# Optimization experiments

Measured on AMD Instinct MI355X. Metric: run time of the kernel, lower is better.

The kernel has to match this reference:

```python
import jax, jax.numpy as jnp
import numpy as np

B, S, H, I, E, K = 2, 2048, 1024, 2816, 8, 2


def setup_inputs() -> dict:
    key = jax.random.key(0)
    k1, k2, k3, k4, k5 = jax.random.split(key, 5)
    std = 0.02
    x = jax.random.normal(k1, (B, S, H), dtype=jnp.float32)
    gate_w = jax.random.normal(k2, (H, E), dtype=jnp.float32) * std   # router Linear(H,E), no bias
    Wg = jax.random.normal(k3, (E, H, I), dtype=jnp.float32) * std    # per-expert gate_proj
    Wu = jax.random.normal(k4, (E, H, I), dtype=jnp.float32) * std    # per-expert up_proj
    Wd = jax.random.normal(k5, (E, I, H), dtype=jnp.float32) * std    # per-expert down_proj
    return {"x": x, "gate_w": gate_w, "Wg": Wg, "Wu": Wu, "Wd": Wd}


def reference(x, gate_w, Wg, Wu, Wd):
    b, s, h = x.shape
    e = gate_w.shape[1]
    # --- Gating ---
    logits = jnp.einsum('bsh,he->bse', x, gate_w)                      # [B,S,E]
    top_vals, top_idx = jax.lax.top_k(logits, K)                       # [B,S,K]
    sel = (top_idx[..., None] == jnp.arange(e)).any(axis=-2)           # [B,S,E] bool, top-k mask
    sparse_logits = jnp.where(sel, logits, -jnp.inf)
    sparse_probs = jax.nn.softmax(sparse_logits, axis=-1)              # zero weight off top-k
    # --- Experts (dense over E, weighted by sparse probs; math identical to gather/scatter loop) ---
    xf = x.reshape(-1, h)                                              # [T,H], T=B*S
    g = jnp.einsum('th,ehi->tei', xf, Wg)                              # [T,E,I]
    u = jnp.einsum('th,ehi->tei', xf, Wu)
    act = jax.nn.silu(g) * u                                           # SwiGLU
    expert_out = jnp.einsum('tei,eih->teh', act, Wd)                   # [T,E,H]
    out = jnp.einsum('teh,te->th', expert_out, sparse_probs.reshape(-1, e))
    final_outputs = out.reshape(b, s, h)
    gate_logit = logits.reshape(-1, e)                                 # [B*S,E]
    return final_outputs, gate_logit
```

## Files before the change

### kernel.cpp

```cpp
#include <hip/hip_runtime.h>


namespace {
constexpr int TOKS = 4096;
constexpr int HDIM = 1024;
constexpr int IDIM = 2816;
constexpr int NEXP = 8;
constexpr int NROW = 8192;

constexpr size_t WGT_OFF = 0;
constexpr size_t WUT_OFF = 46137344;
constexpr size_t WDT_OFF = 92274688;
constexpr size_t A_OFF   = 138412032;
constexpr size_t ACT_OFF = 155189248;
constexpr size_t CNT_OFF = 201326592;
constexpr size_t OFS_OFF = CNT_OFF + 64;
constexpr size_t CUR_OFF = CNT_OFF + 128;
constexpr size_t TIX_OFF = CNT_OFF + 1024;
constexpr size_t TPR_OFF = TIX_OFF + 32768;
constexpr size_t SLT_OFF = TPR_OFF + 32768;
constexpr size_t PRT_OFF = 0;
}

typedef __attribute__((ext_vector_type(8))) short short8;
typedef __attribute__((ext_vector_type(8))) unsigned short ushort8;
typedef __attribute__((ext_vector_type(4))) float f32x4;

__device__ __forceinline__ unsigned short f2bf(float f) {
  union { float f; unsigned int u; } v; v.f = f;
  unsigned int u = v.u;
  return (unsigned short)((u + 0x7fffu + ((u >> 16) & 1u)) >> 16);
}

__device__ __forceinline__ void gl2lds16(const void* g, void* l) {
  __builtin_amdgcn_global_load_lds(
      (const __attribute__((address_space(1))) void*)g,
      (__attribute__((address_space(3))) void*)l, 16, 0, 0);
}

__global__ void k_init(int* __restrict__ cnt) {
  if (threadIdx.x < NEXP) cnt[threadIdx.x] = 0;
}

__global__ __launch_bounds__(256) void k_transpose(
    const float* __restrict__ in, unsigned short* __restrict__ out,
    int R, int C) {
  const size_t eoff = (size_t)blockIdx.z * R * C;
  in += eoff; out += eoff;
  __shared__ float tile[64][65];
  const int c0 = blockIdx.x * 64, r0 = blockIdx.y * 64;
  const int tid = threadIdx.x;
  const int rr = tid >> 4, cc4 = (tid & 15) * 4;
#pragma unroll
  for (int i = 0; i < 4; ++i) {
    int r = rr + i * 16;
    float4 v = *(const float4*)(in + (size_t)(r0 + r) * C + c0 + cc4);
    tile[r][cc4 + 0] = v.x; tile[r][cc4 + 1] = v.y;
    tile[r][cc4 + 2] = v.z; tile[r][cc4 + 3] = v.w;
  }
  __syncthreads();
  const int j = tid & 7;
#pragma unroll
  for (int i = 0; i < 2; ++i) {
    int c = (tid >> 3) + i * 32;
    ushort8 o;
#pragma unroll
    for (int k = 0; k < 8; ++k) o[k] = f2bf(tile[j * 8 + k][c]);
    *(ushort8*)(out + (size_t)(c0 + c) * R + r0 + j * 8) = o;
  }
}

__global__ __launch_bounds__(256) void k_gating(
    const float* __restrict__ x, const float* __restrict__ gw,
    float* __restrict__ logits_out, int* __restrict__ cnt,
    int2* __restrict__ tidx, float2* __restrict__ tprb) {
  const int lane = threadIdx.x & 63;
  const int t = blockIdx.x * 4 + (threadIdx.x >> 6);
  const float* xr = x + (size_t)t * HDIM;
  double acc[8];
#pragma unroll
  for (int e = 0; e < 8; ++e) acc[e] = 0.0;
#pragma unroll
  for (int j = 0; j < 16; ++j) {
    int h = lane + j * 64;
    float xv = xr[h];
    const float4* g = (const float4*)(gw + (size_t)h * 8);
    float4 g0 = g[0], g1 = g[1];
    acc[0] += (double)xv * g0.x; acc[1] += (double)xv * g0.y;
    acc[2] += (double)xv * g0.z; acc[3] += (double)xv * g0.w;
    acc[4] += (double)xv * g1.x; acc[5] += (double)xv * g1.y;
    acc[6] += (double)xv * g1.z; acc[7] += (double)xv * g1.w;
  }
#pragma unroll
  for (int off = 32; off > 0; off >>= 1) {
#pragma unroll
    for (int e = 0; e < 8; ++e) acc[e] += __shfl_down(acc[e], off);
  }
  if (lane == 0) {
    float lg[8];
#pragma unroll
    for (int e = 0; e < 8; ++e) lg[e] = (float)acc[e];
#pragma unroll
    for (int e = 0; e < 8; ++e) logits_out[(size_t)t * 8 + e] = lg[e];
    float v0 = lg[0]; int i0 = 0; float v1 = -3.0e38f; int i1 = 0;
#pragma unroll
    for (int e = 1; e < 8; ++e) {
      if (lg[e] > v0) { v1 = v0; i1 = i0; v0 = lg[e]; i0 = e; }
      else if (lg[e] > v1) { v1 = lg[e]; i1 = e; }
    }
    float ex = expf(v1 - v0);
    float p0 = 1.0f / (1.0f + ex);
    float p1 = ex / (1.0f + ex);
    tidx[t] = make_int2(i0, i1);
    tprb[t] = make_float2(p0, p1);
    atomicAdd(&cnt[i0], 1);
    atomicAdd(&cnt[i1], 1);
  }
}

__global__ void k_prefix(const int* __restrict__ cnt, int* __restrict__ offs,
                         int* __restrict__ cur) {
  if (threadIdx.x == 0) {
    int s = 0;
    for (int e = 0; e < NEXP; ++e) { offs[e] = s; cur[e] = s; s += cnt[e]; }
  }
}

__global__ __launch_bounds__(256) void k_build(
    const float* __restrict__ x, const int2* __restrict__ tidx,
    int* __restrict__ cur, int* __restrict__ slot_row,
    unsigned short* __restrict__ A) {
  const int t = blockIdx.x;
  __shared__ int rs[2];
  if (threadIdx.x == 0) {
    int2 ii = tidx[t];
    int r0 = atomicAdd(&cur[ii.x], 1);
    int r1 = atomicAdd(&cur[ii.y], 1);
    rs[0] = r0; rs[1] = r1;
    slot_row[t * 2] = r0; slot_row[t * 2 + 1] = r1;
  }
  __syncthreads();
  const int r0 = rs[0], r1 = rs[1];
  float4 v = ((const float4*)(x + (size_t)t * HDIM))[threadIdx.x];
  ushort4 b;
  b.x = f2bf(v.x); b.y = f2bf(v.y); b.z = f2bf(v.z); b.w = f2bf(v.w);
  ((ushort4*)(A + (size_t)r0 * HDIM))[threadIdx.x] = b;
  ((ushort4*)(A + (size_t)r1 * HDIM))[threadIdx.x] = b;
}

__global__ __launch_bounds__(256, 2) void k_gemm1(
    const unsigned short* __restrict__ A, const unsigned short* __restrict__ WgT,
    const unsigned short* __restrict__ WuT, unsigned short* __restrict__ act,
    const int* __restrict__ cnt, const int* __restrict__ offs) {
  const int e = blockIdx.z;
  const int ne = cnt[e];
  const int m0 = blockIdx.y * 128;
  if (m0 >= ne) return;
  const int off = offs[e];
  const int n0 = blockIdx.x * 64;
  const unsigned short* Bg = WgT + ((size_t)e * IDIM + n0) * HDIM;
  const unsigned short* Bu = WuT + ((size_t)e * IDIM + n0) * HDIM;

  __shared__ unsigned short As[128 * 64];
  __shared__ unsigned short Bgs[64 * 64];
  __shared__ unsigned short Bus[64 * 64];

  const int tid = threadIdx.x, w = tid >> 6, lane = tid & 63;
  const int lrow8 = lane >> 3;
  const int swz = ((lane & 7) ^ lrow8) * 8;
  const int m16 = lane & 15, quad = lane >> 4, l7 = lane & 7;

  f32x4 accg[2][4], accu[2][4];
#pragma unroll
  for (int mi = 0; mi < 2; ++mi)
#pragma unroll
    for (int ni = 0; ni < 4; ++ni) {
      accg[mi][ni] = (f32x4){0.f, 0.f, 0.f, 0.f};
      accu[mi][ni] = (f32x4){0.f, 0.f, 0.f, 0.f};
    }

  for (int kt = 0; kt < HDIM / 64; ++kt) {
    const int k0 = kt * 64;
#pragma unroll
    for (int i = 0; i < 4; ++i) {
      int gr = off + m0 + w * 32 + i * 8 + lrow8;
      gr = gr > (NROW - 1) ? (NROW - 1) : gr;
      gl2lds16(A + (size_t)gr * HDIM + k0 + swz, &As[(w * 32 + i * 8) * 64]);
    }
#pragma unroll
    for (int i = 0; i < 2; ++i) {
      int rl = w * 16 + i * 8 + lrow8;
      gl2lds16(Bg + (size_t)rl * HDIM + k0 + swz, &Bgs[(w * 16 + i * 8) * 64]);
      gl2lds16(Bu + (size_t)rl * HDIM + k0 + swz, &Bus[(w * 16 + i * 8) * 64]);
    }
    __syncthreads();
#pragma unroll
    for (int kk = 0; kk < 2; ++kk) {
      const int jc = ((kk * 4 + quad) ^ l7) * 8;
      short8 af[2], bgf[4], buf[4];
#pragma unroll
      for (int mi = 0; mi < 2; ++mi)
        af[mi] = *(const short8*)&As[(w * 32 + mi * 16 + m16) * 64 + jc];
#pragma unroll
      for (int ni = 0; ni < 4; ++ni) {
        bgf[ni] = *(const short8*)&Bgs[(ni * 16 + m16) * 64 + jc];
        buf[ni] = *(const short8*)&Bus[(ni * 16 + m16) * 64 + jc];
      }
#pragma unroll
      for (int mi = 0; mi < 2; ++mi)
#pragma unroll
        for (int ni = 0; ni < 4; ++ni) {
          accg[mi][ni] = __builtin_amdgcn_mfma_f32_16x16x32_bf16(
              af[mi], bgf[ni], accg[mi][ni], 0, 0, 0);
          accu[mi][ni] = __builtin_amdgcn_mfma_f32_16x16x32_bf16(
              af[mi], buf[ni], accu[mi][ni], 0, 0, 0);
        }
    }
    __syncthreads();
  }
#pragma unroll
  for (int mi = 0; mi < 2; ++mi)
#pragma unroll
    for (int ni = 0; ni < 4; ++ni)
#pragma unroll
      for (int r = 0; r < 4; ++r) {
        int ml = w * 32 + mi * 16 + quad * 4 + r;
        float g = accg[mi][ni][r];
        float u = accu[mi][ni][r];
        float s = g / (1.0f + __expf(-g));
        As[ml * 64 + ni * 16 + m16] = f2bf(s * u);
      }
  __syncthreads();
#pragma unroll
  for (int i = 0; i < 4; ++i) {
    int chunk = i * 256 + tid;
    int row = chunk >> 3, j = chunk & 7;
    if (m0 + row < ne)
      *(ushort8*)&act[(size_t)(off + m0 + row) * IDIM + n0 + j * 8] =
          *(const ushort8*)&As[row * 64 + j * 8];
  }
}

__global__ __launch_bounds__(256, 2) void k_gemm2(
    const unsigned short* __restrict__ act, const unsigned short* __restrict__ WdT,
    float* __restrict__ partial, const int* __restrict__ cnt,
    const int* __restrict__ offs) {
  const int e = blockIdx.z;
  const int ne = cnt[e];
  const int m0 = blockIdx.y * 128;
  if (m0 >= ne) return;
  const int off = offs[e];
  const int n0 = blockIdx.x * 128;
  const unsigned short* B = WdT + ((size_t)e * HDIM + n0) * IDIM;

  __shared__ unsigned short As[128 * 64];
  __shared__ unsigned short Bs[128 * 64];

  const int tid = threadIdx.x, w = tid >> 6, lane = tid & 63;
  const int lrow8 = lane >> 3;
  const int swz = ((lane & 7) ^ lrow8) * 8;
  const int m16 = lane & 15, quad = lane >> 4, l7 = lane & 7;
  const int wm = (w >> 1) * 64, wn = (w & 1) * 64;

  f32x4 acc[4][4];
#pragma unroll
  for (int mi = 0; mi < 4; ++mi)
#pragma unroll
    for (int ni = 0; ni < 4; ++ni) acc[mi][ni] = (f32x4){0.f, 0.f, 0.f, 0.f};

  for (int kt = 0; kt < IDIM / 64; ++kt) {
    const int k0 = kt * 64;
#pragma unroll
    for (int i = 0; i < 4; ++i) {
      int rl = w * 32 + i * 8 + lrow8;
      int gr = off + m0 + rl;
      gr = gr > (NROW - 1) ? (NROW - 1) : gr;
      gl2lds16(act + (size_t)gr * IDIM + k0 + swz, &As[(w * 32 + i * 8) * 64]);
      gl2lds16(B + (size_t)rl * IDIM + k0 + swz, &Bs[(w * 32 + i * 8) * 64]);
    }
    __syncthreads();
#pragma unroll
    for (int kk = 0; kk < 2; ++kk) {
      const int jc = ((kk * 4 + quad) ^ l7) * 8;
      short8 af[4], bf[4];
#pragma unroll
      for (int mi = 0; mi < 4; ++mi)
        af[mi] = *(const short8*)&As[(wm + mi * 16 + m16) * 64 + jc];
#pragma unroll
      for (int ni = 0; ni < 4; ++ni)
        bf[ni] = *(const short8*)&Bs[(wn + ni * 16 + m16) * 64 + jc];
#pragma unroll
      for (int mi = 0; mi < 4; ++mi)
#pragma unroll
        for (int ni = 0; ni < 4; ++ni)
          acc[mi][ni] = __builtin_amdgcn_mfma_f32_16x16x32_bf16(
              af[mi], bf[ni], acc[mi][ni], 0, 0, 0);
    }
    __syncthreads();
  }
#pragma unroll
  for (int mi = 0; mi < 4; ++mi)
#pragma unroll
    for (int ni = 0; ni < 4; ++ni)
#pragma unroll
      for (int r = 0; r < 4; ++r) {
        int ml = wm + mi * 16 + quad * 4 + r;
        if (m0 + ml < ne)
          partial[(size_t)(off + m0 + ml) * HDIM + n0 + wn + ni * 16 + m16] =
              acc[mi][ni][r];
      }
}

__global__ __launch_bounds__(256) void k_combine(
    const float* __restrict__ partial, const int* __restrict__ slot_row,
    const float2* __restrict__ tprb, float* __restrict__ out) {
  const int t = blockIdx.x;
  const int r0 = slot_row[2 * t], r1 = slot_row[2 * t + 1];
  const float2 p = tprb[t];
  float4 a = ((const float4*)(partial + (size_t)r0 * HDIM))[threadIdx.x];
  float4 b = ((const float4*)(partial + (size_t)r1 * HDIM))[threadIdx.x];
  float4 o;
  o.x = p.x * a.x + p.y * b.x;
  o.y = p.x * a.y + p.y * b.y;
  o.z = p.x * a.z + p.y * b.z;
  o.w = p.x * a.w + p.y * b.w;
  ((float4*)(out + (size_t)t * HDIM))[threadIdx.x] = o;
}

extern "C" void kernel_launch(void* const* d_in, const int* in_sizes, int n_in,
                              void* d_out, int out_size, void* d_ws, size_t ws_size,
                              hipStream_t stream) {
  const float* x  = (const float*)d_in[0];
  const float* gw = (const float*)d_in[1];
  const float* Wg = (const float*)d_in[2];
  const float* Wu = (const float*)d_in[3];
  const float* Wd = (const float*)d_in[4];
  float* out = (float*)d_out;
  char* ws = (char*)d_ws;

  unsigned short* WgT = (unsigned short*)(ws + WGT_OFF);
  unsigned short* WuT = (unsigned short*)(ws + WUT_OFF);
  unsigned short* WdT = (unsigned short*)(ws + WDT_OFF);
  unsigned short* A   = (unsigned short*)(ws + A_OFF);
  unsigned short* act = (unsigned short*)(ws + ACT_OFF);
  float* partial = (float*)(ws + PRT_OFF);
  int* cnt  = (int*)(ws + CNT_OFF);
  int* offs = (int*)(ws + OFS_OFF);
  int* cur  = (int*)(ws + CUR_OFF);
  int2* tidx = (int2*)(ws + TIX_OFF);
  float2* tprb = (float2*)(ws + TPR_OFF);
  int* slot_row = (int*)(ws + SLT_OFF);

  float* logits_out = out + (size_t)TOKS * HDIM;

  k_init<<<1, 64, 0, stream>>>(cnt);
  k_transpose<<<dim3(IDIM / 64, HDIM / 64, NEXP), 256, 0, stream>>>(Wg, WgT, HDIM, IDIM);
  k_transpose<<<dim3(IDIM / 64, HDIM / 64, NEXP), 256, 0, stream>>>(Wu, WuT, HDIM, IDIM);
  k_transpose<<<dim3(HDIM / 64, IDIM / 64, NEXP), 256, 0, stream>>>(Wd, WdT, IDIM, HDIM);
  k_gating<<<TOKS / 4, 256, 0, stream>>>(x, gw, logits_out, cnt, tidx, tprb);
  k_prefix<<<1, 64, 0, stream>>>(cnt, offs, cur);
  k_build<<<TOKS, 256, 0, stream>>>(x, tidx, cur, slot_row, A);
  k_gemm1<<<dim3(IDIM / 64, TOKS / 128, NEXP), 256, 0, stream>>>(A, WgT, WuT, act, cnt, offs);
  k_gemm2<<<dim3(HDIM / 128, TOKS / 128, NEXP), 256, 0, stream>>>(act, WdT, partial, cnt, offs);
  k_combine<<<TOKS, 256, 0, stream>>>(partial, slot_row, tprb, out);
}
```

Baseline: 693.2 us.

## Fuse weight transpose and bf16 conversion into GEMM tile loads

```diff
diff --git a/kernel.cpp b/kernel.cpp
--- a/kernel.cpp
+++ b/kernel.cpp
@@ -8,18 +8,15 @@
 constexpr int NEXP = 8;
 constexpr int NROW = 8192;
 
-constexpr size_t WGT_OFF = 0;
-constexpr size_t WUT_OFF = 46137344;
-constexpr size_t WDT_OFF = 92274688;
-constexpr size_t A_OFF   = 138412032;
-constexpr size_t ACT_OFF = 155189248;
-constexpr size_t CNT_OFF = 201326592;
+constexpr size_t A_OFF   = 0;
+constexpr size_t ACT_OFF = 16777216;
+constexpr size_t PRT_OFF = 62914560;
+constexpr size_t CNT_OFF = 96468992;
 constexpr size_t OFS_OFF = CNT_OFF + 64;
 constexpr size_t CUR_OFF = CNT_OFF + 128;
 constexpr size_t TIX_OFF = CNT_OFF + 1024;
 constexpr size_t TPR_OFF = TIX_OFF + 32768;
 constexpr size_t SLT_OFF = TPR_OFF + 32768;
-constexpr size_t PRT_OFF = 0;
 }
 
 typedef __attribute__((ext_vector_type(8))) short short8;
@@ -38,36 +35,45 @@
       (__attribute__((address_space(3))) void*)l, 16, 0, 0);
 }
 
+struct WT {
+  float4 a, b, c, d;
+};
+
+__device__ __forceinline__ WT load_w64(const float* __restrict__ Wt, int ld,
+                                       int tid) {
+  const int kq = tid >> 4, n4 = (tid & 15) * 4;
+  const float* p = Wt + (size_t)kq * 4 * ld + n4;
+  WT r;
+  r.a = *(const float4*)(p);
+  r.b = *(const float4*)(p + ld);
+  r.c = *(const float4*)(p + 2 * (size_t)ld);
+  r.d = *(const float4*)(p + 3 * (size_t)ld);
+  return r;
+}
+
+__device__ __forceinline__ void store_w64(const WT& r,
+                                          unsigned short* __restrict__ lds,
+                                          int tid) {
+  const int kq = tid >> 4, n4 = (tid & 15) * 4;
+  const int hi16 = kq >> 1, half8 = (kq & 1) * 8;
+  const float* fa = (const float*)&r.a;
+  const float* fb = (const float*)&r.b;
+  const float* fc = (const float*)&r.c;
+  const float* fd = (const float*)&r.d;
+#pragma unroll
+  for (int dn = 0; dn < 4; ++dn) {
+    unsigned int lo = __builtin_amdgcn_perm(
+        __float_as_uint(fb[dn]), __float_as_uint(fa[dn]), 0x07060302u);
+    unsigned int hi = __builtin_amdgcn_perm(
+        __float_as_uint(fd[dn]), __float_as_uint(fc[dn]), 0x07060302u);
+    int row = n4 + dn;
+    int boff = row * 128 + ((hi16 ^ (row & 7)) * 16) + half8;
+    *(uint2*)((char*)lds + boff) = make_uint2(lo, hi);
+  }
+}
+
 __global__ void k_init(int* __restrict__ cnt) {
   if (threadIdx.x < NEXP) cnt[threadIdx.x] = 0;
-}
-
-__global__ __launch_bounds__(256) void k_transpose(
-    const float* __restrict__ in, unsigned short* __restrict__ out,
-    int R, int C) {
-  const size_t eoff = (size_t)blockIdx.z * R * C;
-  in += eoff; out += eoff;
-  __shared__ float tile[64][65];
-  const int c0 = blockIdx.x * 64, r0 = blockIdx.y * 64;
-  const int tid = threadIdx.x;
-  const int rr = tid >> 4, cc4 = (tid & 15) * 4;
-#pragma unroll
-  for (int i = 0; i < 4; ++i) {
-    int r = rr + i * 16;
-    float4 v = *(const float4*)(in + (size_t)(r0 + r) * C + c0 + cc4);
-    tile[r][cc4 + 0] = v.x; tile[r][cc4 + 1] = v.y;
-    tile[r][cc4 + 2] = v.z; tile[r][cc4 + 3] = v.w;
-  }
-  __syncthreads();
-  const int j = tid & 7;
-#pragma unroll
-  for (int i = 0; i < 2; ++i) {
-    int c = (tid >> 3) + i * 32;
-    ushort8 o;
-#pragma unroll
-    for (int k = 0; k < 8; ++k) o[k] = f2bf(tile[j * 8 + k][c]);
-    *(ushort8*)(out + (size_t)(c0 + c) * R + r0 + j * 8) = o;
-  }
 }
 
 __global__ __launch_bounds__(256) void k_gating(
@@ -149,8 +155,8 @@
 }
 
 __global__ __launch_bounds__(256, 2) void k_gemm1(
-    const unsigned short* __restrict__ A, const unsigned short* __restrict__ WgT,
-    const unsigned short* __restrict__ WuT, unsigned short* __restrict__ act,
+    const unsigned short* __restrict__ A, const float* __restrict__ Wg,
+    const float* __restrict__ Wu, unsigned short* __restrict__ act,
     const int* __restrict__ cnt, const int* __restrict__ offs) {
   const int e = blockIdx.z;
   const int ne = cnt[e];
@@ -158,8 +164,8 @@
   if (m0 >= ne) return;
   const int off = offs[e];
   const int n0 = blockIdx.x * 64;
-  const unsigned short* Bg = WgT + ((size_t)e * IDIM + n0) * HDIM;
-  const unsigned short* Bu = WuT + ((size_t)e * IDIM + n0) * HDIM;
+  const float* Bg = Wg + (size_t)e * HDIM * IDIM + n0;
+  const float* Bu = Wu + (size_t)e * HDIM * IDIM + n0;
 
   __shared__ unsigned short As[128 * 64];
   __shared__ unsigned short Bgs[64 * 64];
@@ -181,18 +187,17 @@
 
   for (int kt = 0; kt < HDIM / 64; ++kt) {
     const int k0 = kt * 64;
+    WT rg = load_w64(Bg + (size_t)k0 * IDIM, IDIM, tid);
+    WT ru = load_w64(Bu + (size_t)k0 * IDIM, IDIM, tid);
+    __syncthreads();
 #pragma unroll
     for (int i = 0; i < 4; ++i) {
       int gr = off + m0 + w * 32 + i * 8 + lrow8;
       gr = gr > (NROW - 1) ? (NROW - 1) : gr;
       gl2lds16(A + (size_t)gr * HDIM + k0 + swz, &As[(w * 32 + i * 8) * 64]);
     }
-#pragma unroll
-    for (int i = 0; i < 2; ++i) {
-      int rl = w * 16 + i * 8 + lrow8;
-      gl2lds16(Bg + (size_t)rl * HDIM + k0 + swz, &Bgs[(w * 16 + i * 8) * 64]);
-      gl2lds16(Bu + (size_t)rl * HDIM + k0 + swz, &Bus[(w * 16 + i * 8) * 64]);
-    }
+    store_w64(rg, Bgs, tid);
+    store_w64(ru, Bus, tid);
     __syncthreads();
 #pragma unroll
     for (int kk = 0; kk < 2; ++kk) {
@@ -216,8 +221,8 @@
               af[mi], buf[ni], accu[mi][ni], 0, 0, 0);
         }
     }
-    __syncthreads();
-  }
+  }
+  __syncthreads();
 #pragma unroll
   for (int mi = 0; mi < 2; ++mi)
 #pragma unroll
@@ -242,7 +247,7 @@
 }
 
 __global__ __launch_bounds__(256, 2) void k_gemm2(
-    const unsigned short* __restrict__ act, const unsigned short* __restrict__ WdT,
+    const unsigned short* __restrict__ act, const float* __restrict__ Wd,
     float* __restrict__ partial, const int* __restrict__ cnt,
     const int* __restrict__ offs) {
   const int e = blockIdx.z;
@@ -251,7 +256,7 @@
   if (m0 >= ne) return;
   const int off = offs[e];
   const int n0 = blockIdx.x * 128;
-  const unsigned short* B = WdT + ((size_t)e * HDIM + n0) * IDIM;
+  const float* Bd = Wd + (size_t)e * IDIM * HDIM + n0;
 
   __shared__ unsigned short As[128 * 64];
   __shared__ unsigned short Bs[128 * 64];
@@ -270,14 +275,17 @@
 
   for (int kt = 0; kt < IDIM / 64; ++kt) {
     const int k0 = kt * 64;
+    WT r0 = load_w64(Bd + (size_t)k0 * HDIM, HDIM, tid);
+    WT r1 = load_w64(Bd + (size_t)k0 * HDIM + 64, HDIM, tid);
+    __syncthreads();
 #pragma unroll
     for (int i = 0; i < 4; ++i) {
-      int rl = w * 32 + i * 8 + lrow8;
-      int gr = off + m0 + rl;
+      int gr = off + m0 + w * 32 + i * 8 + lrow8;
       gr = gr > (NROW - 1) ? (NROW - 1) : gr;
       gl2lds16(act + (size_t)gr * IDIM + k0 + swz, &As[(w * 32 + i * 8) * 64]);
-      gl2lds16(B + (size_t)rl * IDIM + k0 + swz, &Bs[(w * 32 + i * 8) * 64]);
-    }
+    }
+    store_w64(r0, Bs, tid);
+    store_w64(r1, Bs + 64 * 64, tid);
     __syncthreads();
 #pragma unroll
     for (int kk = 0; kk < 2; ++kk) {
@@ -296,7 +304,6 @@
           acc[mi][ni] = __builtin_amdgcn_mfma_f32_16x16x32_bf16(
               af[mi], bf[ni], acc[mi][ni], 0, 0, 0);
     }
-    __syncthreads();
   }
 #pragma unroll
   for (int mi = 0; mi < 4; ++mi)
@@ -338,9 +345,6 @@
   float* out = (float*)d_out;
   char* ws = (char*)d_ws;
 
-  unsigned short* WgT = (unsigned short*)(ws + WGT_OFF);
-  unsigned short* WuT = (unsigned short*)(ws + WUT_OFF);
-  unsigned short* WdT = (unsigned short*)(ws + WDT_OFF);
   unsigned short* A   = (unsigned short*)(ws + A_OFF);
   unsigned short* act = (unsigned short*)(ws + ACT_OFF);
   float* partial = (float*)(ws + PRT_OFF);
@@ -354,13 +358,10 @@
   float* logits_out = out + (size_t)TOKS * HDIM;
 
   k_init<<<1, 64, 0, stream>>>(cnt);
-  k_transpose<<<dim3(IDIM / 64, HDIM / 64, NEXP), 256, 0, stream>>>(Wg, WgT, HDIM, IDIM);
-  k_transpose<<<dim3(IDIM / 64, HDIM / 64, NEXP), 256, 0, stream>>>(Wu, WuT, HDIM, IDIM);
-  k_transpose<<<dim3(HDIM / 64, IDIM / 64, NEXP), 256, 0, stream>>>(Wd, WdT, IDIM, HDIM);
   k_gating<<<TOKS / 4, 256, 0, stream>>>(x, gw, logits_out, cnt, tidx, tprb);
   k_prefix<<<1, 64, 0, stream>>>(cnt, offs, cur);
   k_build<<<TOKS, 256, 0, stream>>>(x, tidx, cur, slot_row, A);
-  k_gemm1<<<dim3(IDIM / 64, TOKS / 128, NEXP), 256, 0, stream>>>(A, WgT, WuT, act, cnt, offs);
-  k_gemm2<<<dim3(HDIM / 128, TOKS / 128, NEXP), 256, 0, stream>>>(act, WdT, partial, cnt, offs);
+  k_gemm1<<<dim3(IDIM / 64, TOKS / 128, NEXP), 256, 0, stream>>>(A, Wg, Wu, act, cnt, offs);
+  k_gemm2<<<dim3(HDIM / 128, TOKS / 128, NEXP), 256, 0, stream>>>(act, Wd, partial, cnt, offs);
   k_combine<<<TOKS, 256, 0, stream>>>(partial, slot_row, tprb, out);
 }
```

Measured after the change: 742.6 us. 7.1% more time.
